# Kernel tuning notes

Measured on AMD Instinct MI355X. Metric: run time of the kernel, lower is better.

The kernel has to match this reference:

```python
import jax, jax.numpy as jnp
import numpy as np

B, S, D, H, M = 2, 2048, 1024, 16, 40
DH = D // H  # 64
L = S + M    # kv length after memory concat


def setup_inputs() -> dict:
    key = jax.random.key(0)
    ks = jax.random.split(key, 20)
    s = 1.0 / np.sqrt(D)
    inp = {
        'v': jax.random.normal(ks[0], (B, S, D), jnp.float32),
        'k': jax.random.normal(ks[1], (B, S, D), jnp.float32),
        'q': jax.random.normal(ks[2], (B, S, D), jnp.float32),
        # additive binary mask (1 = masked out), broadcast over heads
        'mask': jax.random.randint(ks[3], (B, 1, S, L), 0, 2).astype(jnp.float32),
        'Wq': jax.random.normal(ks[4], (D, D), jnp.float32) * s,
        'bq': jnp.zeros((D,), jnp.float32),
        'Wk': jax.random.normal(ks[5], (D, D), jnp.float32) * s,
        'bk': jnp.zeros((D,), jnp.float32),
        'Wv': jax.random.normal(ks[6], (D, D), jnp.float32) * s,
        'bv': jnp.zeros((D,), jnp.float32),
        'k_memory': jax.random.normal(ks[7], (1, M, D), jnp.float32) * (1.0 / np.sqrt(DH)),
        'v_memory': jax.random.normal(ks[8], (1, M, D), jnp.float32) * (1.0 / np.sqrt(M)),
        'Wkm': jax.random.normal(ks[9], (D, D), jnp.float32) * s,
        'bkm': jnp.zeros((D,), jnp.float32),
        'Wvm': jax.random.normal(ks[10], (D, D), jnp.float32) * s,
        'bvm': jnp.zeros((D,), jnp.float32),
        'Wo': jax.random.normal(ks[11], (D, D), jnp.float32) * s,
        'bo': jnp.zeros((D,), jnp.float32),
    }
    return inp


def _split_heads(x):
    # [B, T, D] -> [B, H, T, DH]
    b, t, _ = x.shape
    return x.reshape(b, t, H, DH).transpose(0, 2, 1, 3)


def reference(v, k, q, mask, Wq, bq, Wk, bk, Wv, bv, k_memory, v_memory,
              Wkm, bkm, Wvm, bvm, Wo, bo):
    qp = q @ Wq + bq
    kp = k @ Wk + bk
    vp = v @ Wv + bv
    km = (k_memory @ Wkm + bkm)  # [1, M, D]
    vm = (v_memory @ Wvm + bvm)  # [1, M, D]
    kc = jnp.concatenate([kp, jnp.broadcast_to(km, (kp.shape[0], M, D))], axis=1)
    vc = jnp.concatenate([vp, jnp.broadcast_to(vm, (vp.shape[0], M, D))], axis=1)
    qh, kh, vh = _split_heads(qp), _split_heads(kc), _split_heads(vc)
    # scores: [B, H, S, L]
    scores = jnp.einsum('bhqd,bhkd->bhqk', qh, kh) / np.sqrt(DH)
    scores = scores + mask * (-1e9)
    attn = jax.nn.softmax(scores, axis=-1)
    ctx = jnp.einsum('bhqk,bhkd->bhqd', attn, vh)  # [B, H, S, DH]
    ctx = ctx.transpose(0, 2, 1, 3).reshape(ctx.shape[0], S, D)
    out = ctx @ Wo + bo
    return (out, attn)
```

## Files before the change

### kernel.cpp

```cpp
#include <hip/hip_runtime.h>
#include <hip/hip_bf16.h>

typedef __attribute__((ext_vector_type(8))) short short8v;
typedef __attribute__((ext_vector_type(4))) short short4v;
typedef __attribute__((ext_vector_type(4))) float f32x4;

constexpr int B_ = 2, S_ = 2048, H_ = 16, MM_ = 40;
constexpr int L_ = S_ + MM_;
constexpr int LP_ = 2112;
constexpr int NT_ = 33;
constexpr float QSCALE = 0.18033688011112042f;

struct S2 { short hi, lo; };
__device__ __forceinline__ S2 split2(float f) {
    unsigned u = __builtin_bit_cast(unsigned, f);
    short hi = (short)(u >> 16);
    float fh = __builtin_bit_cast(float, u & 0xFFFF0000u);
    float fl = f - fh;
    short lo = (short)(__builtin_bit_cast(unsigned, fl) >> 16);
    return {hi, lo};
}
__device__ __forceinline__ short f2bh(float f) {
    unsigned u = __builtin_bit_cast(unsigned, f);
    u = (u + 0x7FFFu + ((u >> 16) & 1u)) >> 16;
    return (short)u;
}
__device__ __forceinline__ f32x4 mfma16(short8v a, short8v b, f32x4 c) {
    return __builtin_amdgcn_mfma_f32_16x16x32_bf16(a, b, c, 0, 0, 0);
}
__device__ __forceinline__ unsigned cvt_pk_bf16(float a, float b) {
    unsigned r;
    asm("v_cvt_pk_bf16_f32 %0, %1, %2" : "=v"(r) : "v"(a), "v"(b));
    return r;
}

__global__ __launch_bounds__(256) void wsplit6_kernel(
    const float* __restrict__ W0, const float* __restrict__ W1,
    const float* __restrict__ W2, const float* __restrict__ W3,
    const float* __restrict__ W4, const float* __restrict__ W5,
    short* __restrict__ WT)
{
    const float* Ws[6] = {W0, W1, W2, W3, W4, W5};
    const float* W = Ws[blockIdx.z];
    short* WTh = WT + (size_t)blockIdx.z * 2097152;
    short* WTl = WTh + 1048576;
    __shared__ float T[64][68];
    const int t = threadIdx.x;
    const int k0 = blockIdx.x * 64, n0 = blockIdx.y * 64;
    {
        int r = t >> 2, c = (t & 3) * 16;
        const float* src = W + (size_t)(k0 + r) * 1024 + n0 + c;
        *(float4*)&T[r][c + 0]  = *(const float4*)(src + 0);
        *(float4*)&T[r][c + 4]  = *(const float4*)(src + 4);
        *(float4*)&T[r][c + 8]  = *(const float4*)(src + 8);
        *(float4*)&T[r][c + 12] = *(const float4*)(src + 12);
    }
    __syncthreads();
    {
        int n = t >> 2, ks = (t & 3) * 16;
        short8v h0, h1, l0, l1;
#pragma unroll
        for (int j = 0; j < 8; ++j) {
            S2 a = split2(T[ks + j][n]);     h0[j] = a.hi; l0[j] = a.lo;
            S2 b = split2(T[ks + 8 + j][n]); h1[j] = b.hi; l1[j] = b.lo;
        }
        size_t dst = (size_t)(n0 + n) * 1024 + k0 + ks;
        *(short8v*)(WTh + dst) = h0;  *(short8v*)(WTh + dst + 8) = h1;
        *(short8v*)(WTl + dst) = l0;  *(short8v*)(WTl + dst + 8) = l1;
    }
}

template<int ASRC>
__device__ __forceinline__ void gemm_core(
    const float* __restrict__ Af, const short* __restrict__ Ahg,
    const short* __restrict__ Alg, const short* __restrict__ WTh,
    const short* __restrict__ WTl, const float* __restrict__ bias,
    float bscale, float scale,
    short* __restrict__ Oh, short* __restrict__ Ol, float* __restrict__ Of,
    int M, int RPB, int TD, int loff, int omode, int bx, int by,
    int kbeg, int kend)
{
    __shared__ short Ah[128][40];
    __shared__ short Al[128][40];
    __shared__ short Bh[128][40];
    __shared__ short Bl[128][40];
    const int tid = threadIdx.x;
    const int lane = tid & 63, wid = tid >> 6;
    const int wr = wid >> 1, wc = wid & 1;
    const int row0 = by * 128, col0 = bx * 128;
    const int sr = tid >> 1, sc = (tid & 1) << 4;

    f32x4 acc[4][4] = {};

    for (int k0 = kbeg; k0 < kend; k0 += 32) {
        if (ASRC == 0) {
            float f[16];
            int gr = row0 + sr;
            if (gr < M) {
                const float* ap = Af + (size_t)gr * 1024 + k0 + sc;
                float4 a0 = *(const float4*)(ap + 0);
                float4 a1 = *(const float4*)(ap + 4);
                float4 a2 = *(const float4*)(ap + 8);
                float4 a3 = *(const float4*)(ap + 12);
                f[0]=a0.x; f[1]=a0.y; f[2]=a0.z; f[3]=a0.w;
                f[4]=a1.x; f[5]=a1.y; f[6]=a1.z; f[7]=a1.w;
                f[8]=a2.x; f[9]=a2.y; f[10]=a2.z; f[11]=a2.w;
                f[12]=a3.x; f[13]=a3.y; f[14]=a3.z; f[15]=a3.w;
            } else {
#pragma unroll
                for (int j = 0; j < 16; ++j) f[j] = 0.f;
            }
            short8v h0, h1, l0, l1;
#pragma unroll
            for (int j = 0; j < 8; ++j) {
                S2 s = split2(f[j]); h0[j] = s.hi; l0[j] = s.lo;
            }
#pragma unroll
            for (int j = 0; j < 8; ++j) {
                S2 s = split2(f[8 + j]); h1[j] = s.hi; l1[j] = s.lo;
            }
            *(short8v*)&Ah[sr][sc] = h0; *(short8v*)&Ah[sr][sc + 8] = h1;
            *(short8v*)&Al[sr][sc] = l0; *(short8v*)&Al[sr][sc + 8] = l1;
        } else {
            const short* ah = Ahg + (size_t)(row0 + sr) * 1024 + k0 + sc;
            const short* al = Alg + (size_t)(row0 + sr) * 1024 + k0 + sc;
            *(short8v*)&Ah[sr][sc]     = *(const short8v*)ah;
            *(short8v*)&Ah[sr][sc + 8] = *(const short8v*)(ah + 8);
            *(short8v*)&Al[sr][sc]     = *(const short8v*)al;
            *(short8v*)&Al[sr][sc + 8] = *(const short8v*)(al + 8);
        }
        {
            const short* bh = WTh + (size_t)(col0 + sr) * 1024 + k0 + sc;
            const short* bl = WTl + (size_t)(col0 + sr) * 1024 + k0 + sc;
            *(short8v*)&Bh[sr][sc]     = *(const short8v*)bh;
            *(short8v*)&Bh[sr][sc + 8] = *(const short8v*)(bh + 8);
            *(short8v*)&Bl[sr][sc]     = *(const short8v*)bl;
            *(short8v*)&Bl[sr][sc + 8] = *(const short8v*)(bl + 8);
        }
        __syncthreads();
        const int kof = (lane >> 4) << 3;
        const int ar = lane & 15;
        short8v afh[4], afl[4], bfh[4], bfl[4];
#pragma unroll
        for (int i = 0; i < 4; ++i) {
            afh[i] = *(const short8v*)&Ah[wr * 64 + i * 16 + ar][kof];
            afl[i] = *(const short8v*)&Al[wr * 64 + i * 16 + ar][kof];
            bfh[i] = *(const short8v*)&Bh[wc * 64 + i * 16 + ar][kof];
            bfl[i] = *(const short8v*)&Bl[wc * 64 + i * 16 + ar][kof];
        }
#pragma unroll
        for (int i = 0; i < 4; ++i)
#pragma unroll
            for (int j = 0; j < 4; ++j) {
                acc[i][j] = mfma16(afh[i], bfh[j], acc[i][j]);
                acc[i][j] = mfma16(afh[i], bfl[j], acc[i][j]);
                acc[i][j] = mfma16(afl[i], bfh[j], acc[i][j]);
            }
        __syncthreads();
    }

#pragma unroll
    for (int i = 0; i < 4; ++i) {
#pragma unroll
        for (int j = 0; j < 4; ++j) {
            int colb = col0 + wc * 64 + j * 16 + (lane & 15);
            float bv = bias[colb] * bscale;
            int rowb = row0 + wr * 64 + i * 16 + ((lane >> 4) << 2);
            if (omode == 2) {
                if (rowb < M) {
                    int bb = rowb / RPB, tt = rowb % RPB;
                    int hh = colb >> 6, dh = colb & 63;
                    short4v hs;
#pragma unroll
                    for (int r = 0; r < 4; ++r)
                        hs[r] = f2bh((acc[i][j][r] + bv) * scale);
                    size_t dst = ((size_t)(bb * H_ + hh) * 64 + dh) * LP_ + loff + tt;
                    *(short4v*)(Oh + dst) = hs;
                }
            } else {
#pragma unroll
                for (int r = 0; r < 4; ++r) {
                    int row = rowb + r;
                    if (row < M) {
                        float o = (acc[i][j][r] + bv) * scale;
                        int bb = row / RPB, tt = row % RPB;
                        if (omode == 0) {
                            Of[((size_t)bb * TD + loff + tt) * 1024 + colb] = o;
                        } else {
                            int hh = colb >> 6, dh = colb & 63;
                            size_t dst = ((size_t)(bb * H_ + hh) * TD + loff + tt) * 64 + dh;
                            S2 s = split2(o);
                            Oh[dst] = s.hi; Ol[dst] = s.lo;
                        }
                    }
                }
            }
        }
    }
}

__global__ __launch_bounds__(256) void qkv_gemm(
    const float* __restrict__ q_in, const float* __restrict__ k_in,
    const float* __restrict__ v_in, const float* __restrict__ kmem,
    const float* __restrict__ vmem, const short* __restrict__ WT,
    const float* __restrict__ bq, const float* __restrict__ bk,
    const float* __restrict__ bv, const float* __restrict__ bkm,
    const float* __restrict__ bvm,
    short* __restrict__ Qh, short* __restrict__ Ql,
    short* __restrict__ Kh, short* __restrict__ Kl, short* __restrict__ Vh,
    const float* __restrict__ mask, unsigned* __restrict__ mp)
{
    const int z = blockIdx.z;
    if (z == 0) {
        const int blk = blockIdx.y * 8 + blockIdx.x;
        for (int rr = 0; rr < 16; ++rr) {
            const int row = blk * 16 + rr;
            const float* mr = mask + (size_t)row * L_;
            unsigned* orow = mp + (size_t)row * 68;
            for (int wd = threadIdx.x; wd < 66; wd += 256) {
                int l0 = wd * 32;
                unsigned bits = 0u;
                int lim = (wd < 65) ? 32 : 8;
                for (int j = 0; j < lim; j += 4) {
                    float4 m4 = *(const float4*)(mr + l0 + j);
                    bits |= ((unsigned)(m4.x != 0.f)) << (j + 0);
                    bits |= ((unsigned)(m4.y != 0.f)) << (j + 1);
                    bits |= ((unsigned)(m4.z != 0.f)) << (j + 2);
                    bits |= ((unsigned)(m4.w != 0.f)) << (j + 3);
                }
                if (wd == 65) bits |= 0xFFFFFF00u;
                orow[wd] = bits;
            }
        }
        for (int k = threadIdx.x; k < 192; k += 256) {
            int g = blk * 192 + k;
            int rd = g / 24, l = L_ + g % 24;
            Vh[(size_t)rd * LP_ + l] = 0;
        }
        return;
    }
    if (z >= 4) {
        if (blockIdx.y != 0) return;
        const int which = (z - 4) >> 1, b = (z - 4) & 1;
        const float* A = which ? vmem : kmem;
        const short* WTh = WT + (size_t)(3 + which) * 2097152;
        const short* WTl = WTh + 1048576;
        const float* bias = which ? bvm : bkm;
        short* Oh = which ? (Vh + (size_t)b * H_ * 64 * LP_)
                          : (Kh + (size_t)b * H_ * LP_ * 64);
        short* Ol = which ? nullptr : (Kl + (size_t)b * H_ * LP_ * 64);
        gemm_core<0>(A, nullptr, nullptr, WTh, WTl, bias, 1.0f, 1.0f,
                     Oh, Ol, nullptr, 40, 40, LP_, S_, which ? 2 : 1,
                     blockIdx.x, 0, 0, 1024);
        return;
    }
    const int g = z - 1;
    const float* A = (g == 0) ? q_in : (g == 1) ? k_in : v_in;
    const short* WTh = WT + (size_t)g * 2097152;
    const short* WTl = WTh + 1048576;
    const float* bias = (g == 0) ? bq : (g == 1) ? bk : bv;
    float scale = (g == 0) ? QSCALE : 1.0f;
    short* Oh = (g == 0) ? Qh : (g == 1) ? Kh : Vh;
    short* Ol = (g == 0) ? Ql : Kl;
    int omode = (g == 2) ? 2 : 1;
    int TD = (g == 0) ? S_ : LP_;
    gemm_core<0>(A, nullptr, nullptr, WTh, WTl, bias, 1.0f, scale,
                 Oh, Ol, nullptr, 4096, 2048, TD, 0, omode,
                 blockIdx.x, blockIdx.y, 0, 1024);
}

__global__ __launch_bounds__(256) void attn4_kernel(
    const short* __restrict__ Qh, const short* __restrict__ Ql,
    const short* __restrict__ Kh, const short* __restrict__ Kl,
    const short* __restrict__ Vh, const unsigned* __restrict__ mp,
    float* __restrict__ attn, float* __restrict__ invg,
    short* __restrict__ Ch, short* __restrict__ Cl)
{
    __shared__ short KhB[2][64][64];
    __shared__ short KlB[2][64][64];
    __shared__ short VB[64][64];
    __shared__ short Ph[4][16][68];

    const int id = blockIdx.x;
    const int wg = (id & 7) * 64 + (id >> 3);
    const int bh = wg >> 4, qb2 = wg & 15;
    const int b = bh >> 4, h = bh & 15;
    const int lane = threadIdx.x & 63, w = threadIdx.x >> 6;
    const int lq = lane & 15, hi = lane >> 4;
    const int sw = lq & 7;
    const int q0A = qb2 * 128 + w * 16;
    const int q0B = q0A + 64;

    const char* kh_g = (const char*)(Kh + (size_t)bh * LP_ * 64);
    const char* kl_g = (const char*)(Kl + (size_t)bh * LP_ * 64);
    const char* v_g  = (const char*)(Vh + (size_t)bh * 64 * LP_);

    auto stage_k = [&](int buf, int tt) {
#pragma unroll
        for (int i = 0; i < 2; ++i) {
            int o = w * 2048 + i * 1024 + lane * 16;
            int r = o >> 7, c = (o >> 4) & 7;
            int cs = c ^ (r & 7);
            const char* sh = kh_g + (size_t)tt * 8192 + r * 128 + cs * 16;
            const char* sl = kl_g + (size_t)tt * 8192 + r * 128 + cs * 16;
            __builtin_amdgcn_global_load_lds((const void*)sh,
                (void*)((char*)&KhB[buf][0][0] + w * 2048 + i * 1024), 16, 0, 0);
            __builtin_amdgcn_global_load_lds((const void*)sl,
                (void*)((char*)&KlB[buf][0][0] + w * 2048 + i * 1024), 16, 0, 0);
        }
    };
    auto stage_v = [&](int tt) {
#pragma unroll
        for (int i = 0; i < 2; ++i) {
            int o = w * 2048 + i * 1024 + lane * 16;
            int dh = o >> 7, c = (o >> 4) & 7;
            int cs = c ^ (dh & 7);
            const char* src = v_g + (size_t)dh * (LP_ * 2) + (size_t)tt * 128 + cs * 16;
            __builtin_amdgcn_global_load_lds((const void*)src,
                (void*)((char*)&VB[0][0] + w * 2048 + i * 1024), 16, 0, 0);
        }
    };

    const size_t qbA = ((size_t)bh * S_ + q0A + lq) * 64 + hi * 8;
    const size_t qbB = ((size_t)bh * S_ + q0B + lq) * 64 + hi * 8;
    const short8v qh0A = *(const short8v*)(Qh + qbA);
    const short8v qh1A = *(const short8v*)(Qh + qbA + 32);
    const short8v ql0A = *(const short8v*)(Ql + qbA);
    const short8v ql1A = *(const short8v*)(Ql + qbA + 32);
    const short8v qh0B = *(const short8v*)(Qh + qbB);
    const short8v qh1B = *(const short8v*)(Qh + qbB + 32);
    const short8v ql0B = *(const short8v*)(Ql + qbB);
    const short8v ql1B = *(const short8v*)(Ql + qbB + 32);
    const unsigned* mrowA = mp + ((size_t)b * S_ + q0A + lq) * 68;
    const unsigned* mrowB = mp + ((size_t)b * S_ + q0B + lq) * 68;

    const int dr = lane >> 2, dc = lane & 3;
    short* dbaseA = (short*)(attn + ((size_t)bh * S_ + q0A + dr) * L_);
    short* dbaseB = (short*)(attn + ((size_t)bh * S_ + q0B + dr) * L_);

    float smA = 0.f, smB = 0.f;
    f32x4 pvA[4] = {};
    f32x4 pvB[4] = {};

    stage_k(0, 0);
    stage_v(0);
    __syncthreads();

    int cur = 0;
    for (int t = 0; t < NT_; ++t) {
        if (t < NT_ - 1) stage_k(cur ^ 1, t + 1);

        const short8v* kp = (const short8v*)&KhB[cur][0][0];
        const short8v* lp = (const short8v*)&KlB[cur][0][0];
        short8v kh0s[4], kh1s[4], kl0s[4], kl1s[4];
#pragma unroll
        for (int ls = 0; ls < 4; ++ls) {
            const int r = ls * 16 + lq;
            kh0s[ls] = kp[r * 8 + (hi ^ sw)];
            kh1s[ls] = kp[r * 8 + ((hi + 4) ^ sw)];
            kl0s[ls] = lp[r * 8 + (hi ^ sw)];
            kl1s[ls] = lp[r * 8 + ((hi + 4) ^ sw)];
        }
        const unsigned w0A = mrowA[2 * t], w1A = mrowA[2 * t + 1];
#pragma unroll
        for (int ls = 0; ls < 4; ++ls) {
            __builtin_amdgcn_s_setprio(1);
            f32x4 acc = {0.f, 0.f, 0.f, 0.f};
            acc = mfma16(kh0s[ls], qh0A, acc); acc = mfma16(kh1s[ls], qh1A, acc);
            acc = mfma16(kh0s[ls], ql0A, acc); acc = mfma16(kh1s[ls], ql1A, acc);
            acc = mfma16(kl0s[ls], qh0A, acc); acc = mfma16(kl1s[ls], qh1A, acc);
            __builtin_amdgcn_s_setprio(0);
            const unsigned wb = (ls & 2) ? w1A : w0A;
            const int sh = (ls & 1) * 16 + hi * 4;
            float pr[4];
#pragma unroll
            for (int r2 = 0; r2 < 4; ++r2) {
                float e = __builtin_exp2f(acc[r2]);
                pr[r2] = ((wb >> (sh + r2)) & 1u) ? 0.f : e;
            }
            smA += (pr[0] + pr[1]) + (pr[2] + pr[3]);
            *(uint2*)&Ph[w][lq][ls * 16 + hi * 4] =
                uint2{cvt_pk_bf16(pr[0], pr[1]), cvt_pk_bf16(pr[2], pr[3])};
        }
        {
            short8v v0 = *(const short8v*)&Ph[w][dr][dc * 8];
            short8v v1 = *(const short8v*)&Ph[w][dr][32 + dc * 8];
            short* dst = dbaseA + t * 64 + dc * 8;
            if (t < NT_ - 1) { *(short8v*)dst = v0; *(short8v*)(dst + 32) = v1; }
            else { *(short8v*)dst = v0; if (dc == 0) *(short8v*)(dst + 32) = v1; }
        }
        __syncthreads();
        short8v vf0[4], vf1[4];
        {
            const short8v* vp = (const short8v*)&VB[0][0];
#pragma unroll
            for (int j = 0; j < 4; ++j) {
                vf0[j] = vp[(j * 16 + lq) * 8 + (hi ^ sw)];
                vf1[j] = vp[(j * 16 + lq) * 8 + ((hi + 4) ^ sw)];
            }
        }
        {
            const short8v pa0 = *(const short8v*)&Ph[w][lq][hi * 8];
            const short8v pa1 = *(const short8v*)&Ph[w][lq][32 + hi * 8];
            __builtin_amdgcn_s_setprio(1);
#pragma unroll
            for (int j = 0; j < 4; ++j) pvA[j] = mfma16(pa0, vf0[j], pvA[j]);
#pragma unroll
            for (int j = 0; j < 4; ++j) pvA[j] = mfma16(pa1, vf1[j], pvA[j]);
            __builtin_amdgcn_s_setprio(0);
        }
        const unsigned w0B = mrowB[2 * t], w1B = mrowB[2 * t + 1];
#pragma unroll
        for (int ls = 0; ls < 4; ++ls) {
            __builtin_amdgcn_s_setprio(1);
            f32x4 acc = {0.f, 0.f, 0.f, 0.f};
            acc = mfma16(kh0s[ls], qh0B, acc); acc = mfma16(kh1s[ls], qh1B, acc);
            acc = mfma16(kh0s[ls], ql0B, acc); acc = mfma16(kh1s[ls], ql1B, acc);
            acc = mfma16(kl0s[ls], qh0B, acc); acc = mfma16(kl1s[ls], qh1B, acc);
            __builtin_amdgcn_s_setprio(0);
            const unsigned wb = (ls & 2) ? w1B : w0B;
            const int sh = (ls & 1) * 16 + hi * 4;
            float pr[4];
#pragma unroll
            for (int r2 = 0; r2 < 4; ++r2) {
                float e = __builtin_exp2f(acc[r2]);
                pr[r2] = ((wb >> (sh + r2)) & 1u) ? 0.f : e;
            }
            smB += (pr[0] + pr[1]) + (pr[2] + pr[3]);
            *(uint2*)&Ph[w][lq][ls * 16 + hi * 4] =
                uint2{cvt_pk_bf16(pr[0], pr[1]), cvt_pk_bf16(pr[2], pr[3])};
        }
        {
            short8v v0 = *(const short8v*)&Ph[w][dr][dc * 8];
            short8v v1 = *(const short8v*)&Ph[w][dr][32 + dc * 8];
            short* dst = dbaseB + t * 64 + dc * 8;
            if (t < NT_ - 1) { *(short8v*)dst = v0; *(short8v*)(dst + 32) = v1; }
            else { *(short8v*)dst = v0; if (dc == 0) *(short8v*)(dst + 32) = v1; }
        }
        {
            const short8v pa0 = *(const short8v*)&Ph[w][lq][hi * 8];
            const short8v pa1 = *(const short8v*)&Ph[w][lq][32 + hi * 8];
            __builtin_amdgcn_s_setprio(1);
#pragma unroll
            for (int j = 0; j < 4; ++j) pvB[j] = mfma16(pa0, vf0[j], pvB[j]);
#pragma unroll
            for (int j = 0; j < 4; ++j) pvB[j] = mfma16(pa1, vf1[j], pvB[j]);
            __builtin_amdgcn_s_setprio(0);
        }
        __syncthreads();
        if (t < NT_ - 1) stage_v(t + 1);
        cur ^= 1;
    }

    smA += __shfl_xor(smA, 16); smA += __shfl_xor(smA, 32);
    smB += __shfl_xor(smB, 16); smB += __shfl_xor(smB, 32);
    if (lane < 16) {
        invg[(size_t)bh * S_ + q0A + lane] = smA > 0.f ? 1.0f / smA : 0.f;
        invg[(size_t)bh * S_ + q0B + lane] = smB > 0.f ? 1.0f / smB : 0.f;
    }

#pragma unroll
    for (int r = 0; r < 4; ++r) {
        float svA = __shfl(smA, hi * 4 + r);
        float svB = __shfl(smB, hi * 4 + r);
        float ivA = svA > 0.f ? 1.0f / svA : 0.f;
        float ivB = svB > 0.f ? 1.0f / svB : 0.f;
#pragma unroll
        for (int j = 0; j < 4; ++j) {
            size_t dA = ((size_t)b * S_ + q0A + hi * 4 + r) * 1024 + h * 64 + j * 16 + lq;
            S2 sA = split2(pvA[j][r] * ivA);
            Ch[dA] = sA.hi; Cl[dA] = sA.lo;
            size_t dB = ((size_t)b * S_ + q0B + hi * 4 + r) * 1024 + h * 64 + j * 16 + lq;
            S2 sB = split2(pvB[j][r] * ivB);
            Ch[dB] = sB.hi; Cl[dB] = sB.lo;
        }
    }
}

__global__ __launch_bounds__(256) void tail_kernel(
    const short* __restrict__ Ch, const short* __restrict__ Cl,
    const short* __restrict__ WT, const float* __restrict__ bo,
    float* __restrict__ Po0, float* __restrict__ Po1,
    float* __restrict__ attn, const float* __restrict__ invg)
{
    const int blk = blockIdx.x;
    if (blk < 512) {
        const int z = blk >> 8, r = blk & 255;
        const short* WTh = WT + (size_t)5 * 2097152;
        gemm_core<1>(nullptr, Ch, Cl, WTh, WTh + 1048576, bo,
                     z == 0 ? 1.0f : 0.0f, 1.0f,
                     nullptr, nullptr, z == 0 ? Po0 : Po1, 4096, 2048, S_, 0, 0,
                     r & 7, r >> 3, z * 512, z * 512 + 512);
        return;
    }
    const int nb = blk - 512;
    const int lane = threadIdx.x & 63, w = threadIdx.x >> 6;
#pragma unroll 1
    for (int i = 0; i < 8; ++i) {
        const int row = nb * 32 + w * 8 + i;
        const float iv = invg[row];
        float* rowf = attn + (size_t)row * L_;
        unsigned* rw = (unsigned*)rowf;
        unsigned u[17];
#pragma unroll
        for (int it = 0; it < 16; ++it) u[it] = rw[lane + it * 64];
        if (lane < 20) u[16] = rw[lane + 1024];
        asm volatile("s_waitcnt vmcnt(0)" ::: "memory");
#pragma unroll
        for (int it = 0; it < 16; ++it) {
            unsigned uu = u[it];
            float2 v;
            v.x = __builtin_bit_cast(float, uu << 16) * iv;
            v.y = __builtin_bit_cast(float, uu & 0xFFFF0000u) * iv;
            *(float2*)(rowf + 2 * (lane + it * 64)) = v;
        }
        if (lane < 20) {
            unsigned uu = u[16];
            float2 v;
            v.x = __builtin_bit_cast(float, uu << 16) * iv;
            v.y = __builtin_bit_cast(float, uu & 0xFFFF0000u) * iv;
            *(float2*)(rowf + 2 * (lane + 1024)) = v;
        }
    }
}

__global__ __launch_bounds__(256) void add_out(
    const float* __restrict__ Po0, const float* __restrict__ Po1,
    float* __restrict__ outp)
{
    int i = (blockIdx.x * 256 + threadIdx.x) * 4;
    float4 a = *(const float4*)(Po0 + i);
    float4 b = *(const float4*)(Po1 + i);
    a.x += b.x; a.y += b.y; a.z += b.z; a.w += b.w;
    *(float4*)(outp + i) = a;
}

extern "C" void kernel_launch(void* const* d_in, const int* in_sizes, int n_in,
                              void* d_out, int out_size, void* d_ws, size_t ws_size,
                              hipStream_t stream)
{
    const float* v_in = (const float*)d_in[0];
    const float* k_in = (const float*)d_in[1];
    const float* q_in = (const float*)d_in[2];
    const float* mask = (const float*)d_in[3];
    const float* Wq = (const float*)d_in[4];  const float* bq = (const float*)d_in[5];
    const float* Wk = (const float*)d_in[6];  const float* bk = (const float*)d_in[7];
    const float* Wv = (const float*)d_in[8];  const float* bv = (const float*)d_in[9];
    const float* kmem = (const float*)d_in[10];
    const float* vmem = (const float*)d_in[11];
    const float* Wkm = (const float*)d_in[12]; const float* bkm = (const float*)d_in[13];
    const float* Wvm = (const float*)d_in[14]; const float* bvm = (const float*)d_in[15];
    const float* Wo = (const float*)d_in[16];  const float* bo = (const float*)d_in[17];

    char* wsb = (char*)d_ws;
    short* WT  = (short*)(wsb);
    short* Qhb = (short*)(wsb + 25165824);
    short* Qlb = (short*)(wsb + 33554432);
    short* Khb = (short*)(wsb + 41943040);
    short* Klb = (short*)(wsb + 50593792);
    short* Vhb = (short*)(wsb + 59244544);
    short* Chb = (short*)(wsb + 67895296);
    short* Clb = (short*)(wsb + 76283904);
    float* invb = (float*)(wsb + 84672512);
    unsigned* mp = (unsigned*)(wsb + 84934656);
    if (ws_size < 86048768) return;
    float* Po0 = (float*)(wsb + 25165824);
    float* Po1 = (float*)(wsb + 41943040);

    float* outp = (float*)d_out;
    float* attnp = outp + (size_t)B_ * S_ * 1024;

    dim3 blk(256);

    wsplit6_kernel<<<dim3(16, 16, 6), blk, 0, stream>>>(Wq, Wk, Wv, Wkm, Wvm, Wo, WT);

    qkv_gemm<<<dim3(8, 32, 8), blk, 0, stream>>>(
        q_in, k_in, v_in, kmem, vmem, WT, bq, bk, bv, bkm, bvm,
        Qhb, Qlb, Khb, Klb, Vhb, mask, mp);

    attn4_kernel<<<dim3(512), blk, 0, stream>>>(
        Qhb, Qlb, Khb, Klb, Vhb, mp, attnp, invb, Chb, Clb);

    tail_kernel<<<dim3(2560), blk, 0, stream>>>(
        Chb, Clb, WT, bo, Po0, Po1, attnp, invb);

    add_out<<<dim3(4096), blk, 0, stream>>>(Po0, Po1, outp);
}
```

Baseline: 575.3 us.

## Double-buffer V tile in attention and split tail kernel into separate launches

The attention loop now double-buffers the V tile in LDS. The next V tile is prefetched alongside the next K tile, which removes the mid-iteration __syncthreads before the V fragment reads. The combined tail kernel is split into an output GEMM kernel, the add kernel, and a separate attention-normalisation kernel launched last. This adds 8 KB of LDS per block, which could lower occupancy, and adds one extra kernel launch.

```diff
diff --git a/kernel.cpp b/kernel.cpp
--- a/kernel.cpp
+++ b/kernel.cpp
@@ -269,6 +269,30 @@
                  blockIdx.x, blockIdx.y, 0, 1024);
 }
 
+__global__ __launch_bounds__(256) void out_gemm(
+    const short* __restrict__ Ch, const short* __restrict__ Cl,
+    const short* __restrict__ WT, const float* __restrict__ bo,
+    float* __restrict__ Po0, float* __restrict__ Po1)
+{
+    const int z = blockIdx.z;
+    const short* WTh = WT + (size_t)5 * 2097152;
+    gemm_core<1>(nullptr, Ch, Cl, WTh, WTh + 1048576, bo,
+                 z == 0 ? 1.0f : 0.0f, 1.0f,
+                 nullptr, nullptr, z == 0 ? Po0 : Po1, 4096, 2048, S_, 0, 0,
+                 blockIdx.x, blockIdx.y, z * 512, z * 512 + 512);
+}
+
+__global__ __launch_bounds__(256) void add_out(
+    const float* __restrict__ Po0, const float* __restrict__ Po1,
+    float* __restrict__ outp)
+{
+    int i = (blockIdx.x * 256 + threadIdx.x) * 4;
+    float4 a = *(const float4*)(Po0 + i);
+    float4 b = *(const float4*)(Po1 + i);
+    a.x += b.x; a.y += b.y; a.z += b.z; a.w += b.w;
+    *(float4*)(outp + i) = a;
+}
+
 __global__ __launch_bounds__(256) void attn4_kernel(
     const short* __restrict__ Qh, const short* __restrict__ Ql,
     const short* __restrict__ Kh, const short* __restrict__ Kl,
@@ -278,7 +302,7 @@
 {
     __shared__ short KhB[2][64][64];
     __shared__ short KlB[2][64][64];
-    __shared__ short VB[64][64];
+    __shared__ short VB[2][64][64];
     __shared__ short Ph[4][16][68];
 
     const int id = blockIdx.x;
@@ -309,7 +333,7 @@
                 (void*)((char*)&KlB[buf][0][0] + w * 2048 + i * 1024), 16, 0, 0);
         }
     };
-    auto stage_v = [&](int tt) {
+    auto stage_v = [&](int buf, int tt) {
 #pragma unroll
         for (int i = 0; i < 2; ++i) {
             int o = w * 2048 + i * 1024 + lane * 16;
@@ -317,7 +341,7 @@
             int cs = c ^ (dh & 7);
             const char* src = v_g + (size_t)dh * (LP_ * 2) + (size_t)tt * 128 + cs * 16;
             __builtin_amdgcn_global_load_lds((const void*)src,
-                (void*)((char*)&VB[0][0] + w * 2048 + i * 1024), 16, 0, 0);
+                (void*)((char*)&VB[buf][0][0] + w * 2048 + i * 1024), 16, 0, 0);
         }
     };
 
@@ -343,12 +367,15 @@
     f32x4 pvB[4] = {};
 
     stage_k(0, 0);
-    stage_v(0);
+    stage_v(0, 0);
     __syncthreads();
 
     int cur = 0;
     for (int t = 0; t < NT_; ++t) {
-        if (t < NT_ - 1) stage_k(cur ^ 1, t + 1);
+        if (t < NT_ - 1) {
+            stage_k(cur ^ 1, t + 1);
+            stage_v(cur ^ 1, t + 1);
+        }
 
         const short8v* kp = (const short8v*)&KhB[cur][0][0];
         const short8v* lp = (const short8v*)&KlB[cur][0][0];
@@ -360,6 +387,15 @@
             kh1s[ls] = kp[r * 8 + ((hi + 4) ^ sw)];
             kl0s[ls] = lp[r * 8 + (hi ^ sw)];
             kl1s[ls] = lp[r * 8 + ((hi + 4) ^ sw)];
+        }
+        short8v vf0[4], vf1[4];
+        {
+            const short8v* vp = (const short8v*)&VB[cur][0][0];
+#pragma unroll
+            for (int j = 0; j < 4; ++j) {
+                vf0[j] = vp[(j * 16 + lq) * 8 + (hi ^ sw)];
+                vf1[j] = vp[(j * 16 + lq) * 8 + ((hi + 4) ^ sw)];
+            }
         }
         const unsigned w0A = mrowA[2 * t], w1A = mrowA[2 * t + 1];
 #pragma unroll
@@ -389,16 +425,6 @@
             if (t < NT_ - 1) { *(short8v*)dst = v0; *(short8v*)(dst + 32) = v1; }
             else { *(short8v*)dst = v0; if (dc == 0) *(short8v*)(dst + 32) = v1; }
         }
-        __syncthreads();
-        short8v vf0[4], vf1[4];
-        {
-            const short8v* vp = (const short8v*)&VB[0][0];
-#pragma unroll
-            for (int j = 0; j < 4; ++j) {
-                vf0[j] = vp[(j * 16 + lq) * 8 + (hi ^ sw)];
-                vf1[j] = vp[(j * 16 + lq) * 8 + ((hi + 4) ^ sw)];
-            }
-        }
         {
             const short8v pa0 = *(const short8v*)&Ph[w][lq][hi * 8];
             const short8v pa1 = *(const short8v*)&Ph[w][lq][32 + hi * 8];
@@ -448,7 +474,6 @@
             __builtin_amdgcn_s_setprio(0);
         }
         __syncthreads();
-        if (t < NT_ - 1) stage_v(t + 1);
         cur ^= 1;
     }
 
@@ -477,23 +502,10 @@
     }
 }
 
-__global__ __launch_bounds__(256) void tail_kernel(
-    const short* __restrict__ Ch, const short* __restrict__ Cl,
-    const short* __restrict__ WT, const float* __restrict__ bo,
-    float* __restrict__ Po0, float* __restrict__ Po1,
+__global__ __launch_bounds__(256) void norm_attn(
     float* __restrict__ attn, const float* __restrict__ invg)
 {
-    const int blk = blockIdx.x;
-    if (blk < 512) {
-        const int z = blk >> 8, r = blk & 255;
-        const short* WTh = WT + (size_t)5 * 2097152;
-        gemm_core<1>(nullptr, Ch, Cl, WTh, WTh + 1048576, bo,
-                     z == 0 ? 1.0f : 0.0f, 1.0f,
-                     nullptr, nullptr, z == 0 ? Po0 : Po1, 4096, 2048, S_, 0, 0,
-                     r & 7, r >> 3, z * 512, z * 512 + 512);
-        return;
-    }
-    const int nb = blk - 512;
+    const int nb = blockIdx.x;
     const int lane = threadIdx.x & 63, w = threadIdx.x >> 6;
 #pragma unroll 1
     for (int i = 0; i < 8; ++i) {
@@ -522,17 +534,6 @@
             *(float2*)(rowf + 2 * (lane + 1024)) = v;
         }
     }
-}
-
-__global__ __launch_bounds__(256) void add_out(
-    const float* __restrict__ Po0, const float* __restrict__ Po1,
-    float* __restrict__ outp)
-{
-    int i = (blockIdx.x * 256 + threadIdx.x) * 4;
-    float4 a = *(const float4*)(Po0 + i);
-    float4 b = *(const float4*)(Po1 + i);
-    a.x += b.x; a.y += b.y; a.z += b.z; a.w += b.w;
-    *(float4*)(outp + i) = a;
 }
 
 extern "C" void kernel_launch(void* const* d_in, const int* in_sizes, int n_in,
@@ -581,8 +582,8 @@
     attn4_kernel<<<dim3(512), blk, 0, stream>>>(
         Qhb, Qlb, Khb, Klb, Vhb, mp, attnp, invb, Chb, Clb);
 
-    tail_kernel<<<dim3(2560), blk, 0, stream>>>(
-        Chb, Clb, WT, bo, Po0, Po1, attnp, invb);
-
+    out_gemm<<<dim3(8, 32, 2), blk, 0, stream>>>(Chb, Clb, WT, bo, Po0, Po1);
     add_out<<<dim3(4096), blk, 0, stream>>>(Po0, Po1, outp);
-}
+
+    norm_attn<<<dim3(2048), blk, 0, stream>>>(attnp, invb);
+}
```

Measured after the change: 578.3 us. About the same (+0.5%).
